# Performance work log

Measured on AMD Instinct MI355X. Metric: run time of the kernel, lower is better.

## Reference

```python
import jax, jax.numpy as jnp
import numpy as np

D_MODEL = 4096
N_Q_HEAD = 32
N_KV_HEAD = 8
HEAD_DIM = D_MODEL // N_Q_HEAD  # 128
N_REP = N_Q_HEAD // N_KV_HEAD   # 4
B, T = 2, 2048


def _rope_tables(seq_len, head_dim, dtype=jnp.float32):
    # theta_i = 10000^(-2*(i-1)/d) for i=1..d/2  (matches torch.pow(10000, -2*(arange(1,d/2+1)-1)/d))
    i = jnp.arange(head_dim // 2, dtype=dtype)
    theta = jnp.power(10000.0, -2.0 * i / head_dim)
    angles = jnp.outer(jnp.arange(seq_len, dtype=dtype), theta)  # [T, d/2]
    return jnp.cos(angles), jnp.sin(angles)


def _apply_rope(x, cos, sin):
    # x: [B, T, h, HD]; pairs are consecutive elements (view_as_complex semantics)
    B_, T_, h, hd = x.shape
    xp = x.reshape(B_, T_, h, hd // 2, 2)
    xr, xi = xp[..., 0], xp[..., 1]
    c = cos[None, :T_, None, :]
    s = sin[None, :T_, None, :]
    out_r = xr * c - xi * s
    out_i = xr * s + xi * c
    return jnp.stack([out_r, out_i], axis=-1).reshape(B_, T_, h, hd)


def setup_inputs() -> dict:
    key = jax.random.key(0)
    ks = jax.random.split(key, 5)
    scale = 0.02
    x = jax.random.normal(ks[0], (B, T, D_MODEL), dtype=jnp.float32)
    wq = jax.random.normal(ks[1], (D_MODEL, N_Q_HEAD * HEAD_DIM), dtype=jnp.float32) * scale
    wk = jax.random.normal(ks[2], (D_MODEL, N_KV_HEAD * HEAD_DIM), dtype=jnp.float32) * scale
    wv = jax.random.normal(ks[3], (D_MODEL, N_KV_HEAD * HEAD_DIM), dtype=jnp.float32) * scale
    wo = jax.random.normal(ks[4], (N_Q_HEAD * HEAD_DIM, D_MODEL), dtype=jnp.float32) * scale
    # causal mask: 1 where masked (strict upper triangle), per masked_fill(mask==1, -inf)
    attention_mask = jnp.triu(jnp.ones((T, T), dtype=jnp.int32), k=1)
    return {"x": x, "wq": wq, "wk": wk, "wv": wv, "wo": wo, "attention_mask": attention_mask}


def reference(x, wq, wk, wv, wo, attention_mask):
    B_, T_, _ = x.shape
    xq = (x @ wq).reshape(B_, T_, N_Q_HEAD, HEAD_DIM)
    xk = (x @ wk).reshape(B_, T_, N_KV_HEAD, HEAD_DIM)
    xv = (x @ wv).reshape(B_, T_, N_KV_HEAD, HEAD_DIM)

    cos, sin = _rope_tables(T_, HEAD_DIM, x.dtype)
    xq = _apply_rope(xq, cos, sin)
    xk = _apply_rope(xk, cos, sin)

    # GQA: repeat kv heads (training path: no cache)
    xk = jnp.repeat(xk, N_REP, axis=2)  # [B, T, HQ, HD]
    xv = jnp.repeat(xv, N_REP, axis=2)

    q = xq.transpose(0, 2, 1, 3)  # [B, H, T, HD]
    k = xk.transpose(0, 2, 1, 3)
    v = xv.transpose(0, 2, 1, 3)

    scores = jnp.einsum('bhqd,bhkd->bhqk', q, k) / jnp.sqrt(jnp.asarray(HEAD_DIM, x.dtype))
    scores = jnp.where(attention_mask[None, None, :, :] == 1, -jnp.inf, scores)
    probs = jax.nn.softmax(scores, axis=-1)
    out = jnp.einsum('bhqk,bhkd->bhqd', probs, v)
    out = out.transpose(0, 2, 1, 3).reshape(B_, T_, N_Q_HEAD * HEAD_DIM)
    return out @ wo
```

## Files before the change

kernel.cpp:

```cpp
#include <hip/hip_runtime.h>
#include <hip/hip_bf16.h>
#include <math.h>

typedef __hip_bfloat16 bf16;
typedef short bf16x8 __attribute__((ext_vector_type(8)));
typedef float f32x4 __attribute__((ext_vector_type(4)));
typedef float f32x16 __attribute__((ext_vector_type(16)));
typedef unsigned int u32;
typedef unsigned short u16;

#define GLD16(g, l)                                                            \
  __builtin_amdgcn_global_load_lds(                                            \
      (const __attribute__((address_space(1))) void*)(g),                      \
      (__attribute__((address_space(3))) void*)(l), 16, 0, 0)

#define SBAR() __builtin_amdgcn_s_barrier()
#define VMCNT(n) asm volatile("s_waitcnt vmcnt(" #n ")")
#define LGKM0() asm volatile("s_waitcnt lgkmcnt(0)")

__global__ void convert_f32_bf16(const float* __restrict__ in,
                                 bf16* __restrict__ out) {
  size_t i = ((size_t)blockIdx.x * 256 + threadIdx.x) * 4;
  float4 v = *(const float4*)(in + i);
  out[i + 0] = __float2bfloat16(v.x);
  out[i + 1] = __float2bfloat16(v.y);
  out[i + 2] = __float2bfloat16(v.z);
  out[i + 3] = __float2bfloat16(v.w);
}

__global__ void transpose_f32_bf16(const float* __restrict__ in,
                                   bf16* __restrict__ out, int R, int C) {
  __shared__ bf16 tile[32][33];
  int tx = threadIdx.x & 31, ty = threadIdx.x >> 5;
  int c0 = blockIdx.x * 32, r0 = blockIdx.y * 32;
#pragma unroll
  for (int i = 0; i < 32; i += 8)
    tile[ty + i][tx] = __float2bfloat16(in[(size_t)(r0 + ty + i) * C + c0 + tx]);
  __syncthreads();
#pragma unroll
  for (int i = 0; i < 32; i += 8)
    out[(size_t)(c0 + ty + i) * R + r0 + tx] = tile[tx][ty + i];
}

__global__ void transpose_v(const bf16* __restrict__ V, bf16* __restrict__ VT) {
  __shared__ bf16 tile[32][33];
  int s = blockIdx.z, b = s >> 3, kvh = s & 7;
  int t0 = blockIdx.x * 32, d0 = blockIdx.y * 32;
  int tx = threadIdx.x & 31, ty = threadIdx.x >> 5;
#pragma unroll
  for (int i = 0; i < 32; i += 8)
    tile[ty + i][tx] =
        V[(size_t)(b * 2048 + t0 + ty + i) * 6144 + kvh * 128 + d0 + tx];
  __syncthreads();
#pragma unroll
  for (int i = 0; i < 32; i += 8)
    VT[((size_t)s * 128 + d0 + ty + i) * 2048 + t0 + tx] = tile[tx][ty + i];
}

__global__ void rope_table_k(float* __restrict__ tab) {
  int idx = blockIdx.x * 256 + threadIdx.x;
  int t = idx >> 6, i = idx & 63;
  float theta = powf(10000.0f, -2.0f * (float)i / 128.0f);
  float ang = (float)t * theta;
  tab[idx * 2 + 0] = cosf(ang);
  tab[idx * 2 + 1] = sinf(ang);
}

__global__ void rope_apply(bf16* __restrict__ X, const float* __restrict__ tab,
                           int nheads, int rowstride, float omul) {
  size_t idx = (size_t)blockIdx.x * 256 + threadIdx.x;
  int i = (int)(idx & 63);
  size_t rest = idx >> 6;
  int h = (int)(rest % nheads);
  size_t r = rest / nheads;
  int t = (int)(r & 2047);
  float c = tab[(t * 64 + i) * 2 + 0];
  float s = tab[(t * 64 + i) * 2 + 1];
  bf16* p = X + r * (size_t)rowstride + h * 128 + 2 * i;
  float xr = __bfloat162float(p[0]), xi = __bfloat162float(p[1]);
  p[0] = __float2bfloat16((xr * c - xi * s) * omul);
  p[1] = __float2bfloat16((xr * s + xi * c) * omul);
}

template <typename OutT>
__global__ __launch_bounds__(512, 2) void gemm_bt8(const bf16* __restrict__ A,
                                                   const bf16* __restrict__ BT,
                                                   OutT* __restrict__ C, int M,
                                                   int N, int K) {
  __shared__ bf16 AS[2][2][128 * 64];
  __shared__ bf16 BS[2][2][128 * 64];

  const int tid = threadIdx.x;
  const int lane = tid & 63;
  const int w = tid >> 6, wm = w >> 2, wn = w & 3;
  const int lr = lane & 15, hi = lane >> 4;

  int gx = gridDim.x;
  int nwg = gx * gridDim.y;
  int bid = blockIdx.y * gx + blockIdx.x;
  int swz = (bid & 7) * (nwg >> 3) + (bid >> 3);
  const int m0 = (swz / gx) * 256, n0 = (swz % gx) * 256;

  const int NKT = K >> 6;
  const int NI = K >> 7;
  const int srow = tid >> 3;
  const int scol = ((tid & 7) ^ (srow & 7)) << 3;

  f32x4 acc[8][4];
#pragma unroll
  for (int m = 0; m < 8; ++m)
#pragma unroll
    for (int n = 0; n < 4; ++n)
#pragma unroll
      for (int j = 0; j < 4; ++j) acc[m][n][j] = 0.f;

  auto STAGE_A = [&](int buf, int kt) {
    int kk0 = (kt < NKT) ? kt * 64 : 0;
#pragma unroll
    for (int hs = 0; hs < 4; ++hs) {
      int ha = hs >> 1, sa = hs & 1;
      const bf16* g = A + (size_t)(m0 + ha * 128 + sa * 64 + srow) * K + kk0 + scol;
      GLD16(g, &AS[buf][ha][(sa * 64 + srow) * 64 + (tid & 7) * 8]);
    }
  };
  auto STAGE_B = [&](int buf, int kt, int half) {
    int kk0 = (kt < NKT) ? kt * 64 : 0;
#pragma unroll
    for (int sa = 0; sa < 2; ++sa) {
      const bf16* g =
          BT + (size_t)(n0 + half * 128 + sa * 64 + srow) * K + kk0 + scol;
      GLD16(g, &BS[buf][half][(sa * 64 + srow) * 64 + (tid & 7) * 8]);
    }
  };

  bf16x8 bfr[4][2], afA[2][2], afB[2][2];
  auto READ_B = [&](int buf) {
#pragma unroll
    for (int n = 0; n < 4; ++n) {
      int row = (wn & 1) * 64 + n * 16 + lr;
#pragma unroll
      for (int kk = 0; kk < 2; ++kk)
        bfr[n][kk] = *(const bf16x8*)(&BS[buf][wn >> 1]
                                         [row * 64 + (((kk * 4 + hi) ^ (row & 7)) << 3)]);
    }
  };
  auto READ_A_TO = [&](bf16x8(&dst)[2][2], int buf, int q) {
#pragma unroll
    for (int mm = 0; mm < 2; ++mm) {
      int row = (q * 2 + mm) * 16 + lr;
#pragma unroll
      for (int kk = 0; kk < 2; ++kk)
        dst[mm][kk] = *(const bf16x8*)(&AS[buf][wm]
                                          [row * 64 + (((kk * 4 + hi) ^ (row & 7)) << 3)]);
    }
  };

#define MFMA16(q, AF)                                                          \
  do {                                                                         \
    _Pragma("unroll") for (int mm = 0; mm < 2; ++mm)                           \
        _Pragma("unroll") for (int n = 0; n < 4; ++n)                          \
        _Pragma("unroll") for (int kk = 0; kk < 2; ++kk)                       \
            acc[(q) * 2 + mm][n] = __builtin_amdgcn_mfma_f32_16x16x32_bf16(    \
                AF[mm][kk], bfr[n][kk], acc[(q) * 2 + mm][n], 0, 0, 0);        \
  } while (0)

  STAGE_A(0, 0);
  STAGE_B(0, 0, 0); STAGE_B(0, 0, 1);
  STAGE_B(1, 1, 0); STAGE_B(1, 1, 1);
  VMCNT(4);
  SBAR();

  for (int i = 0; i < NI; ++i) {
    int t = 2 * i;
    READ_B(0); READ_A_TO(afA, 0, 0); READ_A_TO(afB, 0, 1);
    STAGE_A(1, t + 1);
    SBAR(); LGKM0();
    __builtin_amdgcn_s_setprio(1); MFMA16(0, afA); MFMA16(1, afB);
    __builtin_amdgcn_s_setprio(0);
    SBAR();
    READ_A_TO(afA, 0, 2); READ_A_TO(afB, 0, 3);
    STAGE_B(0, t + 2, 0); STAGE_B(0, t + 2, 1);
    SBAR(); LGKM0();
    __builtin_amdgcn_s_setprio(1); MFMA16(2, afA); MFMA16(3, afB);
    __builtin_amdgcn_s_setprio(0);
    VMCNT(4);
    SBAR();
    READ_B(1); READ_A_TO(afA, 1, 0); READ_A_TO(afB, 1, 1);
    STAGE_A(0, t + 2);
    SBAR(); LGKM0();
    __builtin_amdgcn_s_setprio(1); MFMA16(0, afA); MFMA16(1, afB);
    __builtin_amdgcn_s_setprio(0);
    SBAR();
    READ_A_TO(afA, 1, 2); READ_A_TO(afB, 1, 3);
    STAGE_B(1, t + 3, 0); STAGE_B(1, t + 3, 1);
    SBAR(); LGKM0();
    __builtin_amdgcn_s_setprio(1); MFMA16(2, afA); MFMA16(3, afB);
    __builtin_amdgcn_s_setprio(0);
    VMCNT(4);
    SBAR();
  }

  VMCNT(0);
  SBAR();

#pragma unroll
  for (int m = 0; m < 8; ++m) {
    int row_base = m0 + wm * 128 + m * 16 + hi * 4;
#pragma unroll
    for (int n = 0; n < 4; ++n) {
      int col = n0 + wn * 64 + n * 16 + lr;
#pragma unroll
      for (int j = 0; j < 4; ++j) {
        float v = acc[m][n][j];
        if constexpr (sizeof(OutT) == 2)
          C[(size_t)(row_base + j) * N + col] = (OutT)__float2bfloat16(v);
        else
          C[(size_t)(row_base + j) * N + col] = (OutT)v;
      }
    }
  }
#undef MFMA16
}

static __device__ inline u32 cvtpk_bf16(float a, float b) {
  u32 r;
  asm("v_cvt_pk_bf16_f32 %0, %1, %2" : "=v"(r) : "v"(a), "v"(b));
  return r;
}

__global__ __launch_bounds__(512) void flash_attn3(const bf16* __restrict__ Q,
                                                   const bf16* __restrict__ K,
                                                   const bf16* __restrict__ VT,
                                                   const float* __restrict__ tab,
                                                   bf16* __restrict__ AO) {
  __shared__ bf16 Kbuf[2][64 * 128];
  __shared__ bf16 Vbuf[2][128 * 64];

  int bid = blockIdx.x;
  int b = bid >> 8;
  int i = (bid >> 3) & 31;
  int kvh = bid & 7;
  int hq = i >> 3;
  int qt = 7 - (i & 7);
  int h = kvh * 4 + hq;

  const int tid = threadIdx.x;
  const int lane = tid & 63, w = tid >> 6;
  const int ql = lane & 31, hi = lane >> 5;
  const int qrow0 = qt * 256 + w * 32;
  const int nt = 4 * qt + 4;

  const bf16* Kg0 = K + (size_t)b * 2048 * 6144 + kvh * 128;
  const bf16* Vg0 = VT + (size_t)(b * 8 + kvh) * 128 * 2048;

  bf16x8 qf[8];
  {
    int tpos = qrow0 + ql;
    const bf16* qb = Q + (size_t)(b * 2048 + tpos) * 6144 + h * 128 + hi * 8;
    const float* tb = tab + (size_t)tpos * 128;
    const float QS = 1.4426950408889634f * 0.08838834764831845f;
#pragma unroll
    for (int dc = 0; dc < 8; ++dc) {
      union { bf16x8 v; u16 s[8]; } in;
      in.v = *(const bf16x8*)(qb + dc * 16);
      union { u32 u[4]; bf16x8 v; } o;
#pragma unroll
      for (int p = 0; p < 4; ++p) {
        int ii = dc * 8 + hi * 4 + p;
        float2 cs = *(const float2*)(tb + 2 * ii);
        float xr = __uint_as_float((u32)in.s[2 * p] << 16);
        float xi = __uint_as_float((u32)in.s[2 * p + 1] << 16);
        o.u[p] = cvtpk_bf16((xr * cs.x - xi * cs.y) * QS,
                            (xr * cs.y + xi * cs.x) * QS);
      }
      qf[dc] = o.v;
    }
  }

  f32x16 O[4];
#pragma unroll
  for (int d4 = 0; d4 < 4; ++d4)
#pragma unroll
    for (int e = 0; e < 16; ++e) O[d4][e] = 0.f;
  float m_ = -1e30f, l_ = 0.f;

  auto STAGE = [&](int buf, int kv0) {
    bf16* Ks = &Kbuf[buf][0];
    bf16* Vs = &Vbuf[buf][0];
    const bf16* Kg = Kg0 + (size_t)kv0 * 6144;
    const bf16* Vg = Vg0 + kv0;
#pragma unroll
    for (int it = 0; it < 2; ++it) {
      int s = it * 512 + tid;
      int row = s >> 4, c = s & 15;
      GLD16(Kg + (size_t)row * 6144 + ((c ^ (row & 7)) << 3), Ks + s * 8);
    }
#pragma unroll
    for (int it = 0; it < 2; ++it) {
      int s = it * 512 + tid;
      int row = s >> 3, c = s & 7;
      GLD16(Vg + (size_t)row * 2048 + ((c ^ (row & 7)) << 3), Vs + s * 8);
    }
  };

  STAGE(0, 0);
  __syncthreads();

  for (int t = 0; t < nt; ++t) {
    int kv0 = t * 64;
    if (t + 1 < nt) STAGE((t + 1) & 1, kv0 + 64);

    if (kv0 <= qrow0 + 31) {
      const bf16* Ks = &Kbuf[t & 1][0];
      const bf16* Vs = &Vbuf[t & 1][0];

      f32x16 Sx[2];
#pragma unroll
      for (int cb = 0; cb < 2; ++cb)
#pragma unroll
        for (int e = 0; e < 16; ++e) Sx[cb][e] = 0.f;

      __builtin_amdgcn_s_setprio(1);
#pragma unroll
      for (int cb = 0; cb < 2; ++cb) {
        int krow = cb * 32 + ql;
#pragma unroll
        for (int dc = 0; dc < 8; ++dc) {
          bf16x8 kf = *(const bf16x8*)(Ks + krow * 128 +
                                       (((dc * 2 + hi) ^ (ql & 7)) << 3));
          Sx[cb] = __builtin_amdgcn_mfma_f32_32x32x16_bf16(kf, qf[dc], Sx[cb],
                                                           0, 0, 0);
        }
      }
      __builtin_amdgcn_s_setprio(0);

      int q = qrow0 + ql;
      bool domask = (kv0 + 63 > qrow0);
      if (domask) {
#pragma unroll
        for (int cb = 0; cb < 2; ++cb)
#pragma unroll
          for (int r = 0; r < 16; ++r) {
            int kv = kv0 + cb * 32 + (r & 3) + 8 * (r >> 2) + 4 * hi;
            if (kv > q) Sx[cb][r] = -1e30f;
          }
      }
      float pm = -1e30f;
#pragma unroll
      for (int cb = 0; cb < 2; ++cb)
#pragma unroll
        for (int r = 0; r < 16; ++r) pm = fmaxf(pm, Sx[cb][r]);
      pm = fmaxf(pm, __shfl_xor(pm, 32));

      if (!__all(pm - m_ <= 11.5416f)) {
        float nm = fmaxf(m_, pm);
        float rs = exp2f(m_ - nm);
        m_ = nm;
        l_ *= rs;
#pragma unroll
        for (int d4 = 0; d4 < 4; ++d4)
#pragma unroll
          for (int e = 0; e < 16; ++e) O[d4][e] *= rs;
      }
      float ps = 0.f;
#pragma unroll
      for (int cb = 0; cb < 2; ++cb)
#pragma unroll
        for (int r = 0; r < 16; ++r) {
          float p = exp2f(Sx[cb][r] - m_);
          Sx[cb][r] = p;
          ps += p;
        }
      ps += __shfl_xor(ps, 32);
      l_ += ps;

      bf16x8 pb[4];
#pragma unroll
      for (int kb = 0; kb < 4; ++kb) {
        int cb = kb >> 1, r0 = 8 * (kb & 1);
        u32 Av = cvtpk_bf16(Sx[cb][r0 + 0], Sx[cb][r0 + 1]);
        u32 Bv = cvtpk_bf16(Sx[cb][r0 + 2], Sx[cb][r0 + 3]);
        u32 Cv = cvtpk_bf16(Sx[cb][r0 + 4], Sx[cb][r0 + 5]);
        u32 Dv = cvtpk_bf16(Sx[cb][r0 + 6], Sx[cb][r0 + 7]);
        u32 sA = (u32)__shfl_xor((int)Av, 32);
        u32 sB = (u32)__shfl_xor((int)Bv, 32);
        u32 sC = (u32)__shfl_xor((int)Cv, 32);
        u32 sD = (u32)__shfl_xor((int)Dv, 32);
        union { u32 u[4]; bf16x8 v; } pk;
        pk.u[0] = hi ? sC : Av;
        pk.u[1] = hi ? sD : Bv;
        pk.u[2] = hi ? Cv : sA;
        pk.u[3] = hi ? Dv : sB;
        pb[kb] = pk.v;
      }

      __builtin_amdgcn_s_setprio(1);
#pragma unroll
      for (int d4 = 0; d4 < 4; ++d4) {
        int vrow = d4 * 32 + ql;
#pragma unroll
        for (int kb = 0; kb < 4; ++kb) {
          bf16x8 vf = *(const bf16x8*)(Vs + vrow * 64 +
                                       (((kb * 2 + hi) ^ (ql & 7)) << 3));
          O[d4] = __builtin_amdgcn_mfma_f32_32x32x16_bf16(vf, pb[kb], O[d4], 0,
                                                          0, 0);
        }
      }
      __builtin_amdgcn_s_setprio(0);
    }
    __syncthreads();
  }

  float inv = 1.0f / l_;
  bf16* outp = AO + (size_t)(b * 2048 + qrow0 + ql) * 4096 + h * 128;
#pragma unroll
  for (int d4 = 0; d4 < 4; ++d4)
#pragma unroll
    for (int rg = 0; rg < 4; ++rg) {
      union { u16 s[4]; unsigned long long v; } pk;
#pragma unroll
      for (int j = 0; j < 4; ++j)
        pk.s[j] = __bfloat16_as_ushort(__float2bfloat16(O[d4][rg * 4 + j] * inv));
      *(unsigned long long*)(outp + d4 * 32 + rg * 8 + hi * 4) = pk.v;
    }
}

extern "C" void kernel_launch(void* const* d_in, const int* in_sizes, int n_in,
                              void* d_out, int out_size, void* d_ws,
                              size_t ws_size, hipStream_t stream) {
  const float* x = (const float*)d_in[0];
  const float* wq = (const float*)d_in[1];
  const float* wk = (const float*)d_in[2];
  const float* wv = (const float*)d_in[3];
  const float* wo = (const float*)d_in[4];

  char* ws = (char*)d_ws;
  bf16* xb    = (bf16*)(ws + 0);
  bf16* WqkvT = (bf16*)(ws + 33554432);
  bf16* WoT   = (bf16*)(ws + 83886080);
  bf16* QKV   = (bf16*)(ws + 117440512);
  bf16* VTb   = (bf16*)(ws + 167772160);
  float* tab  = (float*)(ws + 176160768);
  bf16* AOb   = xb;

  convert_f32_bf16<<<16384, 256, 0, stream>>>(x, xb);
  transpose_f32_bf16<<<dim3(128, 128), 256, 0, stream>>>(wq, WqkvT, 4096, 4096);
  transpose_f32_bf16<<<dim3(32, 128), 256, 0, stream>>>(
      wk, WqkvT + (size_t)4096 * 4096, 4096, 1024);
  transpose_f32_bf16<<<dim3(32, 128), 256, 0, stream>>>(
      wv, WqkvT + (size_t)5120 * 4096, 4096, 1024);
  transpose_f32_bf16<<<dim3(128, 128), 256, 0, stream>>>(wo, WoT, 4096, 4096);
  rope_table_k<<<512, 256, 0, stream>>>(tab);

  gemm_bt8<bf16><<<dim3(24, 16), 512, 0, stream>>>(xb, WqkvT, QKV, 4096, 6144,
                                                   4096);

  rope_apply<<<8192, 256, 0, stream>>>(QKV + 4096, tab, 8, 6144, 1.0f);

  transpose_v<<<dim3(64, 4, 16), 256, 0, stream>>>(QKV + 5120, VTb);

  flash_attn3<<<512, 512, 0, stream>>>(QKV, QKV + 4096, VTb, tab, AOb);

  gemm_bt8<float><<<dim3(16, 16), 512, 0, stream>>>(AOb, WoT, (float*)d_out,
                                                    4096, 4096, 4096);
}
```

Before: 608.0 us.

## Use simpler 128x128 single-buffered GEMM for output projection

Adds a new GEMM kernel with 128x128 tiles, 256 threads, K-step 32 and a single LDS buffer, and uses it for the output projection in place of the double-buffered 256-wide gemm_bt8. The smaller tile gives 1024 workgroups instead of 256, which may fill the GPU better. In exchange it loses the prefetch/compute overlap, performs more global loads per FLOP, and loads LDS with no swizzle, so bank conflicts are possible.

```diff
diff --git a/kernel.cpp b/kernel.cpp
--- a/kernel.cpp
+++ b/kernel.cpp
@@ -80,6 +80,71 @@
   float xr = __bfloat162float(p[0]), xi = __bfloat162float(p[1]);
   p[0] = __float2bfloat16((xr * c - xi * s) * omul);
   p[1] = __float2bfloat16((xr * s + xi * c) * omul);
+}
+
+template <typename OutT>
+__global__ __launch_bounds__(256, 3) void gemm_bt(const bf16* __restrict__ A,
+                                                  const bf16* __restrict__ BT,
+                                                  OutT* __restrict__ C, int M,
+                                                  int N, int K) {
+  __shared__ bf16 As[128 * 32];
+  __shared__ bf16 Bs[128 * 32];
+  const int tid = threadIdx.x;
+  const int lane = tid & 63, w = tid >> 6;
+  const int wr = w >> 1, wc = w & 1;
+  const int lr = lane & 15;
+  const int ko = (lane >> 4) * 8;
+  const int m0 = blockIdx.y * 128, n0 = blockIdx.x * 128;
+
+  f32x4 acc[4][4];
+#pragma unroll
+  for (int m = 0; m < 4; ++m)
+#pragma unroll
+    for (int n = 0; n < 4; ++n)
+#pragma unroll
+      for (int j = 0; j < 4; ++j) acc[m][n][j] = 0.f;
+
+  for (int k0 = 0; k0 < K; k0 += 32) {
+#pragma unroll
+    for (int i = 0; i < 2; ++i) {
+      int c = i * 256 + tid;
+      const bf16* ga = A + (size_t)(m0 + (c >> 2)) * K + k0 + (c & 3) * 8;
+      const bf16* gb = BT + (size_t)(n0 + (c >> 2)) * K + k0 + (c & 3) * 8;
+      GLD16(ga, As + c * 8);
+      GLD16(gb, Bs + c * 8);
+    }
+    __syncthreads();
+    bf16x8 af[4], bfr[4];
+#pragma unroll
+    for (int m = 0; m < 4; ++m)
+      af[m] = *(const bf16x8*)(As + (wr * 64 + m * 16 + lr) * 32 + ko);
+#pragma unroll
+    for (int n = 0; n < 4; ++n)
+      bfr[n] = *(const bf16x8*)(Bs + (wc * 64 + n * 16 + lr) * 32 + ko);
+#pragma unroll
+    for (int m = 0; m < 4; ++m)
+#pragma unroll
+      for (int n = 0; n < 4; ++n)
+        acc[m][n] = __builtin_amdgcn_mfma_f32_16x16x32_bf16(af[m], bfr[n],
+                                                            acc[m][n], 0, 0, 0);
+    __syncthreads();
+  }
+#pragma unroll
+  for (int m = 0; m < 4; ++m) {
+    int row_base = m0 + wr * 64 + m * 16 + (lane >> 4) * 4;
+#pragma unroll
+    for (int n = 0; n < 4; ++n) {
+      int col = n0 + wc * 64 + n * 16 + lr;
+#pragma unroll
+      for (int j = 0; j < 4; ++j) {
+        float v = acc[m][n][j];
+        if constexpr (sizeof(OutT) == 2)
+          C[(size_t)(row_base + j) * N + col] = (OutT)__float2bfloat16(v);
+        else
+          C[(size_t)(row_base + j) * N + col] = (OutT)v;
+      }
+    }
+  }
 }
 
 template <typename OutT>
@@ -461,6 +526,6 @@
 
   flash_attn3<<<512, 512, 0, stream>>>(QKV, QKV + 4096, VTb, tab, AOb);
 
-  gemm_bt8<float><<<dim3(16, 16), 512, 0, stream>>>(AOb, WoT, (float*)d_out,
-                                                    4096, 4096, 4096);
-}
+  gemm_bt<float><<<dim3(32, 32), 256, 0, stream>>>(AOb, WoT, (float*)d_out,
+                                                   4096, 4096, 4096);
+}
```

New measurement: 639.8 us. 5.2% more time.

## Halve flash-attention block size and remap blocks for finer causal load balance

Applied to the files above, without the earlier changes.

The flash attention kernel moves from 512-thread blocks covering 256 query rows to 256-thread blocks covering 128 query rows, with twice as many blocks. The block index is remapped so that consecutive launch slots spread across XCDs and heavy causal tiles are scheduled first. The aim is to reduce tail imbalance and raise occupancy. The cost is that K/V tiles are staged per 128 query rows instead of per 256, so global K/V traffic doubles. The max and sum reductions are also split into four independent accumulators to shorten dependency chains.

```diff
diff --git a/kernel.cpp b/kernel.cpp
--- a/kernel.cpp
+++ b/kernel.cpp
@@ -228,7 +228,7 @@
   return r;
 }
 
-__global__ __launch_bounds__(512) void flash_attn3(const bf16* __restrict__ Q,
+__global__ __launch_bounds__(256) void flash_attn3(const bf16* __restrict__ Q,
                                                    const bf16* __restrict__ K,
                                                    const bf16* __restrict__ VT,
                                                    const float* __restrict__ tab,
@@ -237,18 +237,18 @@
   __shared__ bf16 Vbuf[2][128 * 64];
 
   int bid = blockIdx.x;
-  int b = bid >> 8;
-  int i = (bid >> 3) & 31;
-  int kvh = bid & 7;
-  int hq = i >> 3;
-  int qt = 7 - (i & 7);
+  int lid = (bid & 7) * 128 + (bid >> 3);
+  int qt = 15 - (lid & 15);
+  int hq = (lid >> 4) & 3;
+  int kvh = (lid >> 6) & 7;
+  int b = lid >> 9;
   int h = kvh * 4 + hq;
 
   const int tid = threadIdx.x;
   const int lane = tid & 63, w = tid >> 6;
   const int ql = lane & 31, hi = lane >> 5;
-  const int qrow0 = qt * 256 + w * 32;
-  const int nt = 4 * qt + 4;
+  const int qrow0 = qt * 128 + w * 32;
+  const int nt = 2 * qt + 2;
 
   const bf16* Kg0 = K + (size_t)b * 2048 * 6144 + kvh * 128;
   const bf16* Vg0 = VT + (size_t)(b * 8 + kvh) * 128 * 2048;
@@ -290,14 +290,14 @@
     const bf16* Kg = Kg0 + (size_t)kv0 * 6144;
     const bf16* Vg = Vg0 + kv0;
 #pragma unroll
-    for (int it = 0; it < 2; ++it) {
-      int s = it * 512 + tid;
+    for (int it = 0; it < 4; ++it) {
+      int s = it * 256 + tid;
       int row = s >> 4, c = s & 15;
       GLD16(Kg + (size_t)row * 6144 + ((c ^ (row & 7)) << 3), Ks + s * 8);
     }
 #pragma unroll
-    for (int it = 0; it < 2; ++it) {
-      int s = it * 512 + tid;
+    for (int it = 0; it < 4; ++it) {
+      int s = it * 256 + tid;
       int row = s >> 3, c = s & 7;
       GLD16(Vg + (size_t)row * 2048 + ((c ^ (row & 7)) << 3), Vs + s * 8);
     }
@@ -345,11 +345,17 @@
             if (kv > q) Sx[cb][r] = -1e30f;
           }
       }
-      float pm = -1e30f;
+      float x0 = -1e30f, x1 = -1e30f, x2 = -1e30f, x3 = -1e30f;
 #pragma unroll
       for (int cb = 0; cb < 2; ++cb)
 #pragma unroll
-        for (int r = 0; r < 16; ++r) pm = fmaxf(pm, Sx[cb][r]);
+        for (int r = 0; r < 16; r += 4) {
+          x0 = fmaxf(x0, Sx[cb][r + 0]);
+          x1 = fmaxf(x1, Sx[cb][r + 1]);
+          x2 = fmaxf(x2, Sx[cb][r + 2]);
+          x3 = fmaxf(x3, Sx[cb][r + 3]);
+        }
+      float pm = fmaxf(fmaxf(x0, x1), fmaxf(x2, x3));
       pm = fmaxf(pm, __shfl_xor(pm, 32));
 
       if (!__all(pm - m_ <= 11.5416f)) {
@@ -362,15 +368,20 @@
 #pragma unroll
           for (int e = 0; e < 16; ++e) O[d4][e] *= rs;
       }
-      float ps = 0.f;
+      float s0 = 0.f, s1 = 0.f, s2 = 0.f, s3 = 0.f;
 #pragma unroll
       for (int cb = 0; cb < 2; ++cb)
 #pragma unroll
-        for (int r = 0; r < 16; ++r) {
-          float p = exp2f(Sx[cb][r] - m_);
-          Sx[cb][r] = p;
-          ps += p;
+        for (int r = 0; r < 16; r += 4) {
+          float p0 = exp2f(Sx[cb][r + 0] - m_);
+          float p1 = exp2f(Sx[cb][r + 1] - m_);
+          float p2 = exp2f(Sx[cb][r + 2] - m_);
+          float p3 = exp2f(Sx[cb][r + 3] - m_);
+          Sx[cb][r + 0] = p0; Sx[cb][r + 1] = p1;
+          Sx[cb][r + 2] = p2; Sx[cb][r + 3] = p3;
+          s0 += p0; s1 += p1; s2 += p2; s3 += p3;
         }
+      float ps = (s0 + s1) + (s2 + s3);
       ps += __shfl_xor(ps, 32);
       l_ += ps;
 
@@ -459,7 +470,7 @@
 
   transpose_v<<<dim3(64, 4, 16), 256, 0, stream>>>(QKV + 5120, VTb);
 
-  flash_attn3<<<512, 512, 0, stream>>>(QKV, QKV + 4096, VTb, tab, AOb);
+  flash_attn3<<<1024, 256, 0, stream>>>(QKV, QKV + 4096, VTb, tab, AOb);
 
   gemm_bt8<float><<<dim3(16, 16), 512, 0, stream>>>(AOb, WoT, (float*)d_out,
                                                     4096, 4096, 4096);
```

New measurement: 652.0 us. 1.07x slower.
